# Kernel tuning notes

Hardware: AMD Instinct MI355X
Metric: run time of the kernel (lower is better)

Reference implementation:

```python
import jax, jax.numpy as jnp
import numpy as np

N = 100000        # nodes
E = 1600000       # edges (avg degree 16)
D = 128           # feature dim (in_dim == out_dim)
L = 3             # num_layers
P = 8             # num_parts


def setup_inputs() -> dict:
    key = jax.random.key(0)
    k1, k2, k3, k4, k5, k6 = jax.random.split(key, 6)
    edge_row = jnp.sort(jax.random.randint(k1, (E,), 0, N))
    edge_col = jax.random.randint(k2, (E,), 0, N)
    edge_vals = jax.random.uniform(k3, (E,), dtype=jnp.float32)
    x = jax.random.normal(k4, (N, D), dtype=jnp.float32)
    stacked_params = jax.random.normal(k5, (L, D, D, P), dtype=jnp.float32)
    layer_weights = jax.random.normal(k6, (L, P), dtype=jnp.float32)
    return {"edge_row": edge_row, "edge_col": edge_col, "edge_vals": edge_vals,
            "x": x, "stacked_params": stacked_params, "layer_weights": layer_weights}


def reference(edge_row, edge_col, edge_vals, x, stacked_params, layer_weights):
    n = x.shape[0]
    num_layers = stacked_params.shape[0]
    h = x
    for i in range(num_layers):
        # sparse adj.spmm(h): gather source features, scale by edge value, sum per row
        msg = h[edge_col] * edge_vals[:, None]                       # [E, D]
        ax = jax.ops.segment_sum(msg, edge_row, num_segments=n)      # [N, D]
        # MyLinear: softmax over the num_parts weight, contract parts dim
        w = jax.nn.softmax(layer_weights[i])                         # [P]
        ww = jnp.einsum('oip,p->oi', stacked_params[i], w)           # [D_out, D_in]
        h = ax @ ww.T                                                # [N, D_out]
        if i < num_layers - 1:
            h = jax.nn.relu(h)
    return h
```

## Files before the change

kernel.cpp:

```cpp
#include <hip/hip_runtime.h>
#include <cstdint>

#define D 128
#define P 8
#define L 3

typedef __attribute__((ext_vector_type(8))) _Float16 f16x8;
typedef __attribute__((ext_vector_type(4))) float    f32x4;

__global__ void prep_edges(const int* __restrict__ er, const int* __restrict__ col,
                           const float* __restrict__ vals,
                           int* __restrict__ rp, uint32_t* __restrict__ epk,
                           int n, int e) {
    int i = blockIdx.x * blockDim.x + threadIdx.x;
    if (i >= e) return;
    union { _Float16 h; uint16_t u; } v;
    v.h = (_Float16)vals[i];
    epk[i] = ((uint32_t)col[i] << 15) | (uint32_t)(v.u & 0x7FFFu);

    int cur = er[i];
    if (i == 0) {
        for (int r = 0; r <= cur; r++) rp[r] = 0;
    } else {
        int prev = er[i - 1];
        for (int r = prev + 1; r <= cur; r++) rp[r] = i;
    }
    if (i == e - 1) {
        for (int r = cur + 1; r <= n; r++) rp[r] = e;
    }
}

__global__ void build_ww(const float* __restrict__ sp, const float* __restrict__ lw,
                         _Float16* __restrict__ wwB) {
    int idx = blockIdx.x * blockDim.x + threadIdx.x;
    if (idx >= L * D * D) return;
    int l = idx / (D * D);
    int rem = idx - l * D * D;
    int o = rem / D;
    int i = rem - o * D;
    float wv[P];
    float m = -1e30f;
#pragma unroll
    for (int p = 0; p < P; p++) { wv[p] = lw[l * P + p]; m = fmaxf(m, wv[p]); }
    float s = 0.f;
#pragma unroll
    for (int p = 0; p < P; p++) { wv[p] = __expf(wv[p] - m); s += wv[p]; }
    float inv = 1.0f / s;
    const float* spp = sp + ((size_t)(l * D + o) * D + i) * P;
    float acc = 0.f;
#pragma unroll
    for (int p = 0; p < P; p++) acc += spp[p] * wv[p];
    int kt = i >> 5, kp = i & 31;
    wwB[(((l * 4 + kt) * D + o) << 5) + kp] = (_Float16)(acc * inv);
}

static __device__ __forceinline__ void mfma_store16(const _Float16 (*s_h)[136],
                                                    const _Float16* __restrict__ wwB_l,
                                                    _Float16* __restrict__ y,
                                                    int row0, int n, int tid) {
    const int w = tid >> 6, lane = tid & 63;
    const int quad = lane >> 4, l16 = lane & 15;
    f32x4 acc[2] = {};
#pragma unroll
    for (int kt = 0; kt < 4; kt++) {
        f16x8 af = *(const f16x8*)&s_h[l16][kt * 32 + quad * 8];
#pragma unroll
        for (int c = 0; c < 2; c++) {
            const int ct = w * 2 + c;
            f16x8 bf = *(const f16x8*)&wwB_l[((kt * D + ct * 16 + l16) << 5) + quad * 8];
            acc[c] = __builtin_amdgcn_mfma_f32_16x16x32_f16(af, bf, acc[c], 0, 0, 0);
        }
    }
#pragma unroll
    for (int c = 0; c < 2; c++) {
        const int ct = w * 2 + c;
#pragma unroll
        for (int rg = 0; rg < 4; rg++) {
            int row = row0 + quad * 4 + rg;
            if (row < n) y[row * D + ct * 16 + l16] = (_Float16)acc[c][rg];
        }
    }
}

__global__ __launch_bounds__(256, 8)
void gemm_x32(const float* __restrict__ x, const _Float16* __restrict__ wwB_l,
              _Float16* __restrict__ y, int n) {
    __shared__ _Float16 s_h[16][136];
    const int tid = threadIdx.x;
    const int row0 = blockIdx.x * 16;
    const int c8 = (tid & 15) * 8;
    {
        int r = tid >> 4;
        int row = row0 + r;
        float4 v0 = {}, v1 = {};
        if (row < n) {
            v0 = *(const float4*)&x[row * D + c8];
            v1 = *(const float4*)&x[row * D + c8 + 4];
        }
        f16x8 h;
        h[0] = (_Float16)v0.x; h[1] = (_Float16)v0.y;
        h[2] = (_Float16)v0.z; h[3] = (_Float16)v0.w;
        h[4] = (_Float16)v1.x; h[5] = (_Float16)v1.y;
        h[6] = (_Float16)v1.z; h[7] = (_Float16)v1.w;
        *(f16x8*)&s_h[r][c8] = h;
    }
    __syncthreads();
    mfma_store16(s_h, wwB_l, y, row0, n, tid);
}

template<int NB>
static __device__ __forceinline__ void gather_chunk(float& a0, float& a1,
                                                    const _Float16* __restrict__ y,
                                                    const uint32_t* __restrict__ epk,
                                                    int e, int l2) {
    uint32_t m[NB];
#pragma unroll
    for (int j = 0; j < NB; j++) m[j] = epk[e + j];
    uint32_t g[NB];
#pragma unroll
    for (int j = 0; j < NB; j++) {
        uint32_t off = (m[j] >> 15) * (uint32_t)D + (uint32_t)l2;
        g[j] = *(const uint32_t*)&y[off];
    }
#pragma unroll
    for (int j = 0; j < NB; j++) {
        union { uint32_t u; _Float16 h[2]; } gg; gg.u = g[j];
        union { uint16_t u; _Float16 h; } vv; vv.u = (uint16_t)(m[j] & 0x7FFFu);
        float vf = (float)vv.h;
        a0 += vf * (float)gg.h[0];
        a1 += vf * (float)gg.h[1];
    }
}

static __device__ __forceinline__ void gather_row64(float& a0, float& a1,
                                                    const _Float16* __restrict__ y,
                                                    const uint32_t* __restrict__ epk,
                                                    int e, int e1, int l2) {
    for (; e + 16 <= e1; e += 16) gather_chunk<16>(a0, a1, y, epk, e, l2);
    if (e + 8 <= e1) { gather_chunk<8>(a0, a1, y, epk, e, l2); e += 8; }
    if (e + 4 <= e1) { gather_chunk<4>(a0, a1, y, epk, e, l2); e += 4; }
    for (; e < e1; e++) gather_chunk<1>(a0, a1, y, epk, e, l2);
}

__global__ __launch_bounds__(256, 8)
void fused_layer(const _Float16* __restrict__ yprev, const int* __restrict__ rp,
                 const uint32_t* __restrict__ epk, const _Float16* __restrict__ wwB_l,
                 _Float16* __restrict__ ynext, int n) {
    __shared__ _Float16 s_h[16][136];
    const int tid = threadIdx.x;
    const int lane = tid & 63;
    const int l2 = lane * 2;
    const int w = __builtin_amdgcn_readfirstlane(tid >> 6);
    const int row0 = blockIdx.x * 16;
    const int rbase = row0 + w * 4;
#pragma unroll 1
    for (int q = 0; q < 4; q++) {
        const int r = rbase + q;
        float a0 = 0.f, a1 = 0.f;
        if (r < n) {
            int e  = __builtin_amdgcn_readfirstlane(rp[r]);
            int e1 = __builtin_amdgcn_readfirstlane(rp[r + 1]);
            gather_row64(a0, a1, yprev, epk, e, e1, l2);
        }
        union { uint32_t u; _Float16 h[2]; } o;
        o.h[0] = (_Float16)fmaxf(a0, 0.f);
        o.h[1] = (_Float16)fmaxf(a1, 0.f);
        *(uint32_t*)&s_h[w * 4 + q][l2] = o.u;
    }
    __syncthreads();
    mfma_store16(s_h, wwB_l, ynext, row0, n, tid);
}

__global__ __launch_bounds__(256, 8)
void spmm_f32(const _Float16* __restrict__ y, const int* __restrict__ rp,
              const uint32_t* __restrict__ epk, float* __restrict__ out, int n) {
    const int tid = threadIdx.x;
    const int lane = tid & 63;
    const int l2 = lane * 2;
    const int w = __builtin_amdgcn_readfirstlane(tid >> 6);
    const int rbase = blockIdx.x * 16 + w * 4;
#pragma unroll 1
    for (int q = 0; q < 4; q++) {
        const int r = rbase + q;
        if (r >= n) continue;
        float a0 = 0.f, a1 = 0.f;
        int e  = __builtin_amdgcn_readfirstlane(rp[r]);
        int e1 = __builtin_amdgcn_readfirstlane(rp[r + 1]);
        gather_row64(a0, a1, y, epk, e, e1, l2);
        *(float2*)&out[(size_t)r * D + l2] = make_float2(a0, a1);
    }
}

extern "C" void kernel_launch(void* const* d_in, const int* in_sizes, int n_in,
                              void* d_out, int out_size, void* d_ws, size_t ws_size,
                              hipStream_t stream) {
    const int*   edge_row  = (const int*)d_in[0];
    const int*   edge_col  = (const int*)d_in[1];
    const float* edge_vals = (const float*)d_in[2];
    const float* x         = (const float*)d_in[3];
    const float* sp        = (const float*)d_in[4];
    const float* lw        = (const float*)d_in[5];
    float* out = (float*)d_out;

    const int E_ = in_sizes[0];
    const int N_ = in_sizes[3] / D;

    char* ws = (char*)d_ws;
    int* row_ptr = (int*)ws;
    size_t off = (((size_t)(N_ + 1) * sizeof(int)) + 255) & ~(size_t)255;
    uint32_t* epk = (uint32_t*)(ws + off);
    off += (size_t)E_ * sizeof(uint32_t);
    off = (off + 255) & ~(size_t)255;
    _Float16* wwB = (_Float16*)(ws + off);
    off += (size_t)L * 4 * D * 32 * sizeof(_Float16);
    off = (off + 255) & ~(size_t)255;
    _Float16* bufA = (_Float16*)(ws + off);
    off += (size_t)N_ * D * sizeof(_Float16);
    _Float16* bufB = (_Float16*)(ws + off);

    prep_edges<<<(E_ + 255) / 256, 256, 0, stream>>>(edge_row, edge_col, edge_vals,
                                                     row_ptr, epk, N_, E_);
    build_ww<<<(L * D * D + 255) / 256, 256, 0, stream>>>(sp, lw, wwB);

    const int sblk = (N_ + 15) / 16;
    const int WWL = 4 * D * 32;

    gemm_x32<<<sblk, 256, 0, stream>>>(x, wwB, bufA, N_);
    fused_layer<<<sblk, 256, 0, stream>>>(bufA, row_ptr, epk, wwB + WWL,     bufB, N_);
    fused_layer<<<sblk, 256, 0, stream>>>(bufB, row_ptr, epk, wwB + 2 * WWL, bufA, N_);
    spmm_f32<<<sblk, 256, 0, stream>>>(bufA, row_ptr, epk, out, N_);
}
```

Measured before the change: 317.6 us.

## Store intermediate node features as per-row scaled FP8 to halve gather traffic

Intermediate layer outputs move from fp16 to fp8 (e4m3) with one fp32 scale per row. Each scale comes from a shared-memory atomicMax over the row's absolute maxima after the MFMA. The SpMM gathers then read 2 bytes per lane plus one scale per edge, instead of 4 bytes, which cuts random-access memory traffic. The cost is an extra scale load per edge, an extra block barrier, conversion arithmetic, and a real loss of accuracy that may threaten the tolerance.

```diff
diff --git a/kernel.cpp b/kernel.cpp
--- a/kernel.cpp
+++ b/kernel.cpp
@@ -7,6 +7,44 @@
 
 typedef __attribute__((ext_vector_type(8))) _Float16 f16x8;
 typedef __attribute__((ext_vector_type(4))) float    f32x4;
+typedef __attribute__((ext_vector_type(2))) float    f32x2;
+
+#if __has_builtin(__builtin_amdgcn_cvt_pk_f32_fp8) && __has_builtin(__builtin_amdgcn_cvt_pk_fp8_f32)
+#define HAVE_FP8_CVT 1
+#else
+#define HAVE_FP8_CVT 0
+#endif
+
+static __device__ __forceinline__ f32x2 fp8x2_to_f32(uint32_t u) {
+#if HAVE_FP8_CVT
+    return __builtin_amdgcn_cvt_pk_f32_fp8((int)u, false);
+#else
+    f32x2 r;
+#pragma unroll
+    for (int i = 0; i < 2; i++) {
+        uint32_t b = (u >> (8 * i)) & 0xffu;
+        uint32_t mag = b & 0x7fu;
+        uint16_t h = (uint16_t)(((b & 0x80u) << 8) | ((mag >= 8u) ? ((mag << 7) + 0x2000u) : 0u));
+        union { uint16_t q; _Float16 hf; } c; c.q = h;
+        r[i] = (float)c.hf;
+    }
+    return r;
+#endif
+}
+
+static __device__ __forceinline__ uint32_t f32_to_fp8(float v) {
+#if HAVE_FP8_CVT
+    return (uint32_t)__builtin_amdgcn_cvt_pk_fp8_f32(v, v, 0, false) & 0xffu;
+#else
+    union { _Float16 hf; uint16_t q; } c; c.hf = (_Float16)v;
+    uint32_t s = ((uint32_t)c.q >> 8) & 0x80u;
+    int t = (int)(c.q & 0x7fff) - 0x2000;
+    if (t < 0) return s;
+    int r = (t + 63 + ((t >> 7) & 1)) >> 7;
+    if (r > 0x7e) r = 0x7e;
+    return s | (uint32_t)r;
+#endif
+}
 
 __global__ void prep_edges(const int* __restrict__ er, const int* __restrict__ col,
                            const float* __restrict__ vals,
@@ -54,10 +92,12 @@
     wwB[(((l * 4 + kt) * D + o) << 5) + kp] = (_Float16)(acc * inv);
 }
 
-static __device__ __forceinline__ void mfma_store16(const _Float16 (*s_h)[136],
-                                                    const _Float16* __restrict__ wwB_l,
-                                                    _Float16* __restrict__ y,
-                                                    int row0, int n, int tid) {
+static __device__ __forceinline__ void mfma_store16_q8(const _Float16 (*s_h)[136],
+                                                       const _Float16* __restrict__ wwB_l,
+                                                       uint8_t* __restrict__ y8,
+                                                       float* __restrict__ scl,
+                                                       unsigned* srow,
+                                                       int row0, int n, int tid) {
     const int w = tid >> 6, lane = tid & 63;
     const int quad = lane >> 4, l16 = lane & 15;
     f32x4 acc[2] = {};
@@ -72,23 +112,41 @@
         }
     }
 #pragma unroll
-    for (int c = 0; c < 2; c++) {
-        const int ct = w * 2 + c;
-#pragma unroll
-        for (int rg = 0; rg < 4; rg++) {
-            int row = row0 + quad * 4 + rg;
-            if (row < n) y[row * D + ct * 16 + l16] = (_Float16)acc[c][rg];
+    for (int rg = 0; rg < 4; rg++) {
+        float m = fmaxf(fabsf(acc[0][rg]), fabsf(acc[1][rg]));
+#pragma unroll
+        for (int d = 1; d < 16; d <<= 1) m = fmaxf(m, __shfl_xor(m, d));
+        if (l16 == 0) atomicMax(&srow[quad * 4 + rg], __float_as_uint(m));
+    }
+    __syncthreads();
+#pragma unroll
+    for (int rg = 0; rg < 4; rg++) {
+        const int rr = quad * 4 + rg;
+        const int row = row0 + rr;
+        float rmax = fmaxf(__uint_as_float(srow[rr]), 1e-20f);
+        float qs = 448.f / rmax;
+        if (row < n) {
+#pragma unroll
+            for (int c = 0; c < 2; c++) {
+                const int ct = w * 2 + c;
+                float v = acc[c][rg] * qs;
+                v = fminf(fmaxf(v, -448.f), 448.f);
+                y8[row * D + ct * 16 + l16] = (uint8_t)f32_to_fp8(v);
+            }
+            if (w == 0 && l16 == 0) scl[row] = rmax * (1.f / 448.f);
         }
     }
 }
 
 __global__ __launch_bounds__(256, 8)
 void gemm_x32(const float* __restrict__ x, const _Float16* __restrict__ wwB_l,
-              _Float16* __restrict__ y, int n) {
+              uint8_t* __restrict__ y8, float* __restrict__ scl, int n) {
     __shared__ _Float16 s_h[16][136];
+    __shared__ unsigned srow[16];
     const int tid = threadIdx.x;
     const int row0 = blockIdx.x * 16;
     const int c8 = (tid & 15) * 8;
+    if (tid < 16) srow[tid] = 0;
     {
         int r = tid >> 4;
         int row = row0 + r;
@@ -105,54 +163,60 @@
         *(f16x8*)&s_h[r][c8] = h;
     }
     __syncthreads();
-    mfma_store16(s_h, wwB_l, y, row0, n, tid);
+    mfma_store16_q8(s_h, wwB_l, y8, scl, srow, row0, n, tid);
 }
 
 template<int NB>
 static __device__ __forceinline__ void gather_chunk(float& a0, float& a1,
-                                                    const _Float16* __restrict__ y,
+                                                    const uint8_t* __restrict__ y8,
                                                     const uint32_t* __restrict__ epk,
+                                                    const float* __restrict__ scl,
                                                     int e, int l2) {
     uint32_t m[NB];
 #pragma unroll
     for (int j = 0; j < NB; j++) m[j] = epk[e + j];
+    float sc[NB];
+#pragma unroll
+    for (int j = 0; j < NB; j++) sc[j] = scl[m[j] >> 15];
     uint32_t g[NB];
 #pragma unroll
+    for (int j = 0; j < NB; j++)
+        g[j] = *(const uint16_t*)&y8[(m[j] >> 15) * (uint32_t)D + (uint32_t)l2];
+#pragma unroll
     for (int j = 0; j < NB; j++) {
-        uint32_t off = (m[j] >> 15) * (uint32_t)D + (uint32_t)l2;
-        g[j] = *(const uint32_t*)&y[off];
-    }
-#pragma unroll
-    for (int j = 0; j < NB; j++) {
-        union { uint32_t u; _Float16 h[2]; } gg; gg.u = g[j];
         union { uint16_t u; _Float16 h; } vv; vv.u = (uint16_t)(m[j] & 0x7FFFu);
-        float vf = (float)vv.h;
-        a0 += vf * (float)gg.h[0];
-        a1 += vf * (float)gg.h[1];
+        float vf = (float)vv.h * sc[j];
+        f32x2 p = fp8x2_to_f32(g[j]);
+        a0 += vf * p[0];
+        a1 += vf * p[1];
     }
 }
 
 static __device__ __forceinline__ void gather_row64(float& a0, float& a1,
-                                                    const _Float16* __restrict__ y,
+                                                    const uint8_t* __restrict__ y8,
                                                     const uint32_t* __restrict__ epk,
+                                                    const float* __restrict__ scl,
                                                     int e, int e1, int l2) {
-    for (; e + 16 <= e1; e += 16) gather_chunk<16>(a0, a1, y, epk, e, l2);
-    if (e + 8 <= e1) { gather_chunk<8>(a0, a1, y, epk, e, l2); e += 8; }
-    if (e + 4 <= e1) { gather_chunk<4>(a0, a1, y, epk, e, l2); e += 4; }
-    for (; e < e1; e++) gather_chunk<1>(a0, a1, y, epk, e, l2);
+    for (; e + 16 <= e1; e += 16) gather_chunk<16>(a0, a1, y8, epk, scl, e, l2);
+    if (e + 8 <= e1) { gather_chunk<8>(a0, a1, y8, epk, scl, e, l2); e += 8; }
+    if (e + 4 <= e1) { gather_chunk<4>(a0, a1, y8, epk, scl, e, l2); e += 4; }
+    for (; e < e1; e++) gather_chunk<1>(a0, a1, y8, epk, scl, e, l2);
 }
 
 __global__ __launch_bounds__(256, 8)
-void fused_layer(const _Float16* __restrict__ yprev, const int* __restrict__ rp,
-                 const uint32_t* __restrict__ epk, const _Float16* __restrict__ wwB_l,
-                 _Float16* __restrict__ ynext, int n) {
+void fused_layer(const uint8_t* __restrict__ yprev, const float* __restrict__ sprev,
+                 const int* __restrict__ rp, const uint32_t* __restrict__ epk,
+                 const _Float16* __restrict__ wwB_l,
+                 uint8_t* __restrict__ ynext, float* __restrict__ snext, int n) {
     __shared__ _Float16 s_h[16][136];
+    __shared__ unsigned srow[16];
     const int tid = threadIdx.x;
     const int lane = tid & 63;
     const int l2 = lane * 2;
     const int w = __builtin_amdgcn_readfirstlane(tid >> 6);
     const int row0 = blockIdx.x * 16;
     const int rbase = row0 + w * 4;
+    if (tid < 16) srow[tid] = 0;
 #pragma unroll 1
     for (int q = 0; q < 4; q++) {
         const int r = rbase + q;
@@ -160,7 +224,7 @@
         if (r < n) {
             int e  = __builtin_amdgcn_readfirstlane(rp[r]);
             int e1 = __builtin_amdgcn_readfirstlane(rp[r + 1]);
-            gather_row64(a0, a1, yprev, epk, e, e1, l2);
+            gather_row64(a0, a1, yprev, epk, sprev, e, e1, l2);
         }
         union { uint32_t u; _Float16 h[2]; } o;
         o.h[0] = (_Float16)fmaxf(a0, 0.f);
@@ -168,12 +232,13 @@
         *(uint32_t*)&s_h[w * 4 + q][l2] = o.u;
     }
     __syncthreads();
-    mfma_store16(s_h, wwB_l, ynext, row0, n, tid);
+    mfma_store16_q8(s_h, wwB_l, ynext, snext, srow, row0, n, tid);
 }
 
 __global__ __launch_bounds__(256, 8)
-void spmm_f32(const _Float16* __restrict__ y, const int* __restrict__ rp,
-              const uint32_t* __restrict__ epk, float* __restrict__ out, int n) {
+void spmm_f32(const uint8_t* __restrict__ y8, const float* __restrict__ sprev,
+              const int* __restrict__ rp, const uint32_t* __restrict__ epk,
+              float* __restrict__ out, int n) {
     const int tid = threadIdx.x;
     const int lane = tid & 63;
     const int l2 = lane * 2;
@@ -186,7 +251,7 @@
         float a0 = 0.f, a1 = 0.f;
         int e  = __builtin_amdgcn_readfirstlane(rp[r]);
         int e1 = __builtin_amdgcn_readfirstlane(rp[r + 1]);
-        gather_row64(a0, a1, y, epk, e, e1, l2);
+        gather_row64(a0, a1, y8, epk, sprev, e, e1, l2);
         *(float2*)&out[(size_t)r * D + l2] = make_float2(a0, a1);
     }
 }
@@ -214,9 +279,14 @@
     _Float16* wwB = (_Float16*)(ws + off);
     off += (size_t)L * 4 * D * 32 * sizeof(_Float16);
     off = (off + 255) & ~(size_t)255;
-    _Float16* bufA = (_Float16*)(ws + off);
-    off += (size_t)N_ * D * sizeof(_Float16);
-    _Float16* bufB = (_Float16*)(ws + off);
+    uint8_t* y8A = (uint8_t*)(ws + off);
+    off += (size_t)N_ * D;
+    uint8_t* y8B = (uint8_t*)(ws + off);
+    off += (size_t)N_ * D;
+    off = (off + 255) & ~(size_t)255;
+    float* scA = (float*)(ws + off);
+    off += (size_t)N_ * sizeof(float);
+    float* scB = (float*)(ws + off);
 
     prep_edges<<<(E_ + 255) / 256, 256, 0, stream>>>(edge_row, edge_col, edge_vals,
                                                      row_ptr, epk, N_, E_);
@@ -225,8 +295,8 @@
     const int sblk = (N_ + 15) / 16;
     const int WWL = 4 * D * 32;
 
-    gemm_x32<<<sblk, 256, 0, stream>>>(x, wwB, bufA, N_);
-    fused_layer<<<sblk, 256, 0, stream>>>(bufA, row_ptr, epk, wwB + WWL,     bufB, N_);
-    fused_layer<<<sblk, 256, 0, stream>>>(bufB, row_ptr, epk, wwB + 2 * WWL, bufA, N_);
-    spmm_f32<<<sblk, 256, 0, stream>>>(bufA, row_ptr, epk, out, N_);
-}
+    gemm_x32<<<sblk, 256, 0, stream>>>(x, wwB, y8A, scA, N_);
+    fused_layer<<<sblk, 256, 0, stream>>>(y8A, scA, row_ptr, epk, wwB + WWL,     y8B, scB, N_);
+    fused_layer<<<sblk, 256, 0, stream>>>(y8B, scB, row_ptr, epk, wwB + 2 * WWL, y8A, scA, N_);
+    spmm_f32<<<sblk, 256, 0, stream>>>(y8A, scA, row_ptr, epk, out, N_);
+}
```

New measurement: 295.9 us. 6.8% less time.
